# Performance work log

Hardware: AMD Instinct MI355X
Metric: run time of the kernel (lower is better)

Reference implementation:

```python
import jax, jax.numpy as jnp
import numpy as np

N = 262144      # total nodes
E = 1048576     # total edges
G = 8192        # num graphs (= batch[-1]+1)
H = 128         # hidden
L = 4           # layers
VA = 64         # atom feature vocab
VB = 8          # bond feature vocab
FA = 9          # atom feature columns
FB = 3          # bond feature columns
BN_EPS = 1e-5


def _bn(x, g, b, m, v):
    # BatchNorm1d in eval mode: running stats
    return (x - m) * jax.lax.rsqrt(v + BN_EPS) * g + b


def setup_inputs() -> dict:
    key = jax.random.key(0)
    ks = jax.random.split(key, 40)
    rn = lambda k, s, sc=0.05: jax.random.normal(k, s, dtype=jnp.float32) * sc
    x = jax.random.randint(ks[0], (N, FA), 0, VA)
    edge_index = jax.random.randint(ks[1], (2, E), 0, N)
    edge_attr = jax.random.randint(ks[2], (E, FB), 0, VB)
    batch = jnp.sort(jax.random.randint(ks[3], (N,), 0, G))
    batch = batch.at[0].set(0).at[-1].set(G - 1)
    params = dict(
        atom_emb=rn(ks[4], (FA, VA, H)),
        vn_emb=rn(ks[5], (H,)),
        bond_emb=rn(ks[6], (L, FB, VB, H)),
        conv_eps=rn(ks[7], (L,)),
        conv_W1=rn(ks[8], (L, H, 2 * H)), conv_b1=rn(ks[9], (L, 2 * H)),
        conv_bn_g=1.0 + rn(ks[10], (L, 2 * H)), conv_bn_b=rn(ks[11], (L, 2 * H)),
        conv_bn_m=rn(ks[12], (L, 2 * H), 0.1),
        conv_bn_v=0.5 + jax.random.uniform(ks[13], (L, 2 * H)) * 0.5,
        conv_W2=rn(ks[14], (L, 2 * H, H)), conv_b2=rn(ks[15], (L, H)),
        vn1_W=rn(ks[16], (L, 2 * H, 2 * H)), vn1_b=rn(ks[17], (L, 2 * H)),
        vn1_g=1.0 + rn(ks[18], (L, 2 * H)), vn1_be=rn(ks[19], (L, 2 * H)),
        vn1_m=rn(ks[20], (L, 2 * H), 0.1),
        vn1_v=0.5 + jax.random.uniform(ks[21], (L, 2 * H)) * 0.5,
        vn2_W=rn(ks[22], (L, 2 * H, H)), vn2_b=rn(ks[23], (L, H)),
        vn2_g=1.0 + rn(ks[24], (L, H)), vn2_be=rn(ks[25], (L, H)),
        vn2_m=rn(ks[26], (L, H), 0.1),
        vn2_v=0.5 + jax.random.uniform(ks[27], (L, H)) * 0.5,
        pW1=rn(ks[28], (H, H)), pb1=rn(ks[29], (H,)),
        pW2=rn(ks[30], (H, 1)), pb2=rn(ks[31], (1,)),
    )
    return dict(x=x, edge_index=edge_index, edge_attr=edge_attr, batch=batch, **params)


def reference(x, edge_index, edge_attr, batch, atom_emb, vn_emb, bond_emb,
              conv_eps, conv_W1, conv_b1, conv_bn_g, conv_bn_b, conv_bn_m, conv_bn_v,
              conv_W2, conv_b2, vn1_W, vn1_b, vn1_g, vn1_be, vn1_m, vn1_v,
              vn2_W, vn2_b, vn2_g, vn2_be, vn2_m, vn2_v, pW1, pb1, pW2, pb2):
    src, dst = edge_index[0], edge_index[1]
    # AtomEncoder: sum of per-feature embeddings -> [N, H]
    h = atom_emb[jnp.arange(FA)[:, None], x.T].sum(0)
    # virtual node embedding broadcast to all graphs: [G, H]
    vn = jnp.broadcast_to(vn_emb, (G, H))
    for i in range(L):
        h = h + vn[batch]
        # CombConv (GIN-with-edge-features): msg = relu(x_j + bond_emb)
        e = bond_emb[i][jnp.arange(FB)[:, None], edge_attr.T].sum(0)  # [E, H]
        msg = jax.nn.relu(h[src] + e)
        agg = jax.ops.segment_sum(msg, dst, num_segments=N)  # [N, H]
        z = (1.0 + conv_eps[i]) * h + agg
        z = jax.nn.relu(_bn(z @ conv_W1[i] + conv_b1[i],
                            conv_bn_g[i], conv_bn_b[i], conv_bn_m[i], conv_bn_v[i]))
        h = z @ conv_W2[i] + conv_b2[i]
        # virtual node update: gather-concat-MLP, pool, MLP
        t = jnp.concatenate([vn[batch], h], axis=-1)  # [N, 2H]
        t = jax.nn.relu(_bn(t @ vn1_W[i] + vn1_b[i],
                            vn1_g[i], vn1_be[i], vn1_m[i], vn1_v[i]))
        pooled = jax.ops.segment_sum(t, batch, num_segments=G)  # [G, 2H]
        vn = jax.nn.relu(_bn(pooled @ vn2_W[i] + vn2_b[i],
                             vn2_g[i], vn2_be[i], vn2_m[i], vn2_v[i]))
    # JK='L': last virtual-node representation; dropout=0
    out = jax.nn.relu(vn @ pW1 + pb1) @ pW2 + pb2  # [G, 1]
    return jnp.clip(out, 0.0, 50.0)  # eval-mode clamp
```

## Files before the change

### kernel.cpp

```cpp
#include <hip/hip_runtime.h>
#include <hip/hip_fp16.h>

#define NN 262144
#define EE 1048576
#define GG 8192
#define HH 128
#define FBc 3
#define VAc 64
#define VBc 8
#define FAc 9

typedef _Float16 f16;
typedef _Float16 f16x8 __attribute__((ext_vector_type(8)));
typedef float f32x4 __attribute__((ext_vector_type(4)));

__device__ __forceinline__ float h2f(ushort u) {
    __half h; *(ushort*)&h = u; return __half2float(h);
}
__device__ __forceinline__ ushort f2h(float f) {
    __half h = __float2half_rn(f); return *(ushort*)&h;
}

__global__ void k_zero(float* __restrict__ p) {
    size_t i = (size_t)(blockIdx.x * 256 + threadIdx.x) * 4;
    *(float4*)(p + i) = make_float4(0.f, 0.f, 0.f, 0.f);
}

__global__ void k_atom(const int* __restrict__ x, const float* __restrict__ emb,
                       ushort* __restrict__ h16) {
    int t = blockIdx.x * 256 + threadIdx.x;
    int n = t >> 5, c = (t & 31) << 2;
    if (n >= NN) return;
    float4 a = make_float4(0.f, 0.f, 0.f, 0.f);
#pragma unroll
    for (int f = 0; f < FAc; ++f) {
        int v = x[n * FAc + f];
        float4 e = *(const float4*)(emb + ((size_t)(f * VAc + v)) * HH + c);
        a.x += e.x; a.y += e.y; a.z += e.z; a.w += e.w;
    }
    ushort4 o;
    o.x = f2h(a.x * 0.0625f); o.y = f2h(a.y * 0.0625f);
    o.z = f2h(a.z * 0.0625f); o.w = f2h(a.w * 0.0625f);
    *(ushort4*)(h16 + (size_t)n * HH + c) = o;
}

__global__ void k_init_vn(const float* __restrict__ vn_emb, float* __restrict__ vn) {
    int t = blockIdx.x * 256 + threadIdx.x;
    int g = t >> 5, c = (t & 31) << 2;
    *(float4*)(vn + (size_t)g * HH + c) = *(const float4*)(vn_emb + c);
}

__global__ void k_hist(const int* __restrict__ ei, int* __restrict__ deg) {
    int e = blockIdx.x * 256 + threadIdx.x;
    atomicAdd(&deg[ei[EE + e]], 1);
}
__global__ void k_scan1(const int* __restrict__ deg, int* __restrict__ rowptr,
                        int* __restrict__ sums) {
    __shared__ int s[256];
    int base = blockIdx.x * 1024 + threadIdx.x * 4;
    int4 d = *(const int4*)(deg + base);
    int t = d.x + d.y + d.z + d.w;
    s[threadIdx.x] = t;
    __syncthreads();
    for (int off = 1; off < 256; off <<= 1) {
        int v = (threadIdx.x >= off) ? s[threadIdx.x - off] : 0;
        __syncthreads();
        s[threadIdx.x] += v;
        __syncthreads();
    }
    int excl = s[threadIdx.x] - t;
    int4 o; o.x = excl; o.y = excl + d.x; o.z = o.y + d.y; o.w = o.z + d.z;
    *(int4*)(rowptr + base) = o;
    if (threadIdx.x == 255) sums[blockIdx.x] = s[255];
}
__global__ void k_scan2(int* __restrict__ sums) {
    __shared__ int s[256];
    int t = sums[threadIdx.x];
    s[threadIdx.x] = t;
    __syncthreads();
    for (int off = 1; off < 256; off <<= 1) {
        int v = (threadIdx.x >= off) ? s[threadIdx.x - off] : 0;
        __syncthreads();
        s[threadIdx.x] += v;
        __syncthreads();
    }
    sums[threadIdx.x] = s[threadIdx.x] - t;
}
__global__ void k_scan3(int* __restrict__ rowptr, const int* __restrict__ sums,
                        int* __restrict__ fill) {
    int base = blockIdx.x * 1024 + threadIdx.x * 4;
    int add = sums[blockIdx.x];
    int4 r = *(const int4*)(rowptr + base);
    r.x += add; r.y += add; r.z += add; r.w += add;
    *(int4*)(rowptr + base) = r;
    *(int4*)(fill + base) = r;
    if (blockIdx.x == 0 && threadIdx.x == 0) rowptr[NN] = EE;
}
__global__ void k_scatter(const int* __restrict__ ei, const int* __restrict__ ea,
                          int* __restrict__ fill, unsigned* __restrict__ packed) {
    int e = blockIdx.x * 256 + threadIdx.x;
    int dst = ei[EE + e];
    int pos = atomicAdd(&fill[dst], 1);
    unsigned cb = (unsigned)(ea[e * 3 + 0] + ea[e * 3 + 1] * 8 + ea[e * 3 + 2] * 64);
    packed[pos] = (unsigned)ei[e] | (cb << 18);
}

__global__ void k_ctab(const float* __restrict__ bemb, float* __restrict__ ctab) {
    int t = blockIdx.x * 256 + threadIdx.x;
    int cb = t >> 5, c = (t & 31) << 2;
    int a0 = cb & 7, a1 = (cb >> 3) & 7, a2 = cb >> 6;
    float4 b0 = *(const float4*)(bemb + (size_t)(0 * VBc + a0) * HH + c);
    float4 b1 = *(const float4*)(bemb + (size_t)(1 * VBc + a1) * HH + c);
    float4 b2 = *(const float4*)(bemb + (size_t)(2 * VBc + a2) * HH + c);
    float4 o = make_float4(b0.x + b1.x + b2.x, b0.y + b1.y + b2.y,
                           b0.z + b1.z + b2.z, b0.w + b1.w + b2.w);
    *(float4*)(ctab + (size_t)cb * HH + c) = o;
}

__global__ void k_prep(const float* __restrict__ b1, const float* __restrict__ g1,
                       const float* __restrict__ be1, const float* __restrict__ m1,
                       const float* __restrict__ v1,
                       const float* __restrict__ g3, const float* __restrict__ be3,
                       const float* __restrict__ m3, const float* __restrict__ v3,
                       float* __restrict__ ZA, float* __restrict__ ZB,
                       float* __restrict__ TA, float* __restrict__ TB,
                       float* __restrict__ S3) {
    int c = threadIdx.x;
    float s1 = g1[c] * rsqrtf(v1[c] + 1e-5f);
    ZA[c] = s1;
    ZB[c] = ((b1[c] - m1[c]) * s1 + be1[c]) * 0.0625f;
    float s3 = g3[c] * rsqrtf(v3[c] + 1e-5f);
    TA[c] = 16.f * s3;
    TB[c] = be3[c] - m3[c] * s3;
    S3[c] = s3;
}

__global__ void k_wt(const float* __restrict__ W, ushort* __restrict__ Wt, int lk, int Nsrc) {
    int o = blockIdx.x * 256 + threadIdx.x;
    int K = 1 << lk;
    int c = o >> lk, k = o & (K - 1);
    Wt[o] = f2h(W[(size_t)k * Nsrc + c]);
}

__global__ void k_agg(const ushort* __restrict__ h16, const float* __restrict__ vn,
                      const int* __restrict__ batch,
                      const int* __restrict__ rowptr, const unsigned* __restrict__ packed,
                      const float* __restrict__ ctab, ushort* __restrict__ agg) {
    int n = blockIdx.x * 4 + (threadIdx.x >> 6);
    int lane = threadIdx.x & 63;
    int co = lane * 2;
    int beg = rowptr[n], end = rowptr[n + 1];
    float a0 = 0.f, a1 = 0.f;
    int i = beg;
    for (; i + 1 < end; i += 2) {
        unsigned p0 = packed[i], p1 = packed[i + 1];
        int s0 = p0 & 0x3FFFF, s1 = p1 & 0x3FFFF;
        int c0 = p0 >> 18, c1 = p1 >> 18;
        ushort2 u0 = *(const ushort2*)(h16 + (size_t)s0 * HH + co);
        ushort2 u1 = *(const ushort2*)(h16 + (size_t)s1 * HH + co);
        float2 v0 = *(const float2*)(vn + (size_t)batch[s0] * HH + co);
        float2 v1 = *(const float2*)(vn + (size_t)batch[s1] * HH + co);
        float2 t0 = *(const float2*)(ctab + (size_t)c0 * HH + co);
        float2 t1 = *(const float2*)(ctab + (size_t)c1 * HH + co);
        a0 += fmaxf(16.f * h2f(u0.x) + v0.x + t0.x, 0.f)
            + fmaxf(16.f * h2f(u1.x) + v1.x + t1.x, 0.f);
        a1 += fmaxf(16.f * h2f(u0.y) + v0.y + t0.y, 0.f)
            + fmaxf(16.f * h2f(u1.y) + v1.y + t1.y, 0.f);
    }
    if (i < end) {
        unsigned p = packed[i];
        int src = p & 0x3FFFF, cb = p >> 18;
        ushort2 u = *(const ushort2*)(h16 + (size_t)src * HH + co);
        float2 vv = *(const float2*)(vn + (size_t)batch[src] * HH + co);
        float2 ct = *(const float2*)(ctab + (size_t)cb * HH + co);
        a0 += fmaxf(16.f * h2f(u.x) + vv.x + ct.x, 0.f);
        a1 += fmaxf(16.f * h2f(u.y) + vv.y + ct.y, 0.f);
    }
    ushort2 o; o.x = f2h(a0 * 0.0625f); o.y = f2h(a1 * 0.0625f);
    *(ushort2*)(agg + (size_t)n * HH + co) = o;
}

__global__ void __launch_bounds__(512)
k_conv(ushort* __restrict__ h16, const ushort* __restrict__ agg,
       const ushort* __restrict__ W1t, const ushort* __restrict__ W2t,
       const ushort* __restrict__ W3t,
       const int* __restrict__ batch, const float* __restrict__ vn,
       const float* __restrict__ vnW,
       const float* __restrict__ eps_ptr,
       const float* __restrict__ ZA, const float* __restrict__ ZB,
       const float* __restrict__ b2,
       const float* __restrict__ TA, const float* __restrict__ TB,
       float* __restrict__ pooled) {
    __shared__ ushort As[128][128];
    __shared__ ushort zs[128][256];
    __shared__ ushort Wb[128][128];
    __shared__ int batchL[128];
    const int tid = threadIdx.x;
    const int r0 = blockIdx.x * 128;
    const int w = tid >> 6, l = tid & 63, lr = l & 15, lg = l >> 4, lr7 = lr & 7;
    if (tid < 128) batchL[tid] = batch[r0 + tid];
    const float eps1 = 1.f + eps_ptr[0];

    {
        int row = w * 16 + (l >> 2), q = l & 3, r7 = row & 7;
        int gg = batch[r0 + row];
        const ushort* hp = h16 + (size_t)(r0 + row) * HH;
        const float* vp = vn + (size_t)gg * HH;
        const ushort* ap = agg + (size_t)(r0 + row) * HH;
#pragma unroll
        for (int j4 = 0; j4 < 4; ++j4) {
            int c0 = q * 32 + j4 * 8;
            f16x8 hv = *(const f16x8*)(hp + c0);
            float4 v0 = *(const float4*)(vp + c0);
            float4 v1 = *(const float4*)(vp + c0 + 4);
            f16x8 ag = *(const f16x8*)(ap + c0);
            float vv[8] = {v0.x, v0.y, v0.z, v0.w, v1.x, v1.y, v1.z, v1.w};
            f16x8 o;
#pragma unroll
            for (int j = 0; j < 8; ++j)
                o[j] = (f16)(eps1 * ((float)hv[j] + vv[j] * 0.0625f) + (float)ag[j]);
            *(f16x8*)&As[row][((c0 >> 3) ^ r7) << 3] = o;
        }
    }

    f32x4 acc[8];
    for (int ch = 0; ch < 2; ++ch) {
        if (ch) __syncthreads();
        {
            int c = tid >> 2, q = tid & 3, c7 = c & 7;
#pragma unroll
            for (int j4 = 0; j4 < 4; ++j4) {
                int blk = q * 4 + j4;
                *(f16x8*)&Wb[c][(blk ^ c7) << 3] =
                    *(const f16x8*)(W1t + (size_t)(ch * 128 + c) * 128 + blk * 8);
            }
        }
        __syncthreads();
#pragma unroll
        for (int fc = 0; fc < 8; ++fc) acc[fc] = (f32x4){0.f, 0.f, 0.f, 0.f};
#pragma unroll
        for (int k0 = 0; k0 < 4; ++k0) {
            int sb = ((k0 * 4 + lg) ^ lr7) << 3;
            f16x8 af = *(const f16x8*)&As[w * 16 + lr][sb];
#pragma unroll
            for (int fc = 0; fc < 8; ++fc) {
                f16x8 bf = *(const f16x8*)&Wb[fc * 16 + lr][sb];
                acc[fc] = __builtin_amdgcn_mfma_f32_16x16x32_f16(af, bf, acc[fc], 0, 0, 0);
            }
        }
#pragma unroll
        for (int fc = 0; fc < 8; ++fc) {
            int col = ch * 128 + fc * 16 + lr;
            float za = ZA[col], zb = ZB[col];
#pragma unroll
            for (int reg = 0; reg < 4; ++reg) {
                int rl = w * 16 + lg * 4 + reg;
                float zv = fmaxf(acc[fc][reg] * za + zb, 0.f);
                ((ushort*)zs)[rl * 256 + ((((col >> 3) ^ (rl & 7)) << 3) | (col & 7))] = f2h(zv);
            }
        }
    }

    for (int ch2 = 0; ch2 < 2; ++ch2) {
        __syncthreads();
        {
            int c = tid >> 3, q = tid & 7, c7 = c & 7;
#pragma unroll
            for (int j4 = 0; j4 < 4; ++j4) {
                int blk = q * 4 + j4;
                *(f16x8*)((ushort*)Wb + c * 256 + ((blk ^ c7) << 3)) =
                    *(const f16x8*)(W2t + (size_t)(ch2 * 64 + c) * 256 + blk * 8);
            }
        }
        __syncthreads();
#pragma unroll
        for (int fc = 0; fc < 4; ++fc) acc[fc] = (f32x4){0.f, 0.f, 0.f, 0.f};
#pragma unroll
        for (int k0 = 0; k0 < 8; ++k0) {
            int sb = ((k0 * 4 + lg) ^ lr7) << 3;
            f16x8 af = *(const f16x8*)&zs[w * 16 + lr][sb];
#pragma unroll
            for (int fc = 0; fc < 4; ++fc) {
                f16x8 bf = *(const f16x8*)((ushort*)Wb + (fc * 16 + lr) * 256 + sb);
                acc[fc] = __builtin_amdgcn_mfma_f32_16x16x32_f16(af, bf, acc[fc], 0, 0, 0);
            }
        }
#pragma unroll
        for (int fc = 0; fc < 4; ++fc) {
            int col = ch2 * 64 + fc * 16 + lr;
            float bb = b2[col];
#pragma unroll
            for (int reg = 0; reg < 4; ++reg) {
                int rl = w * 16 + lg * 4 + reg;
                float hv = acc[fc][reg] * 16.f + bb;
                ushort hq = f2h(hv * 0.0625f);
                h16[(size_t)(r0 + rl) * HH + col] = hq;
                As[rl][(((col >> 3) ^ (rl & 7)) << 3) | (col & 7)] = hq;
            }
        }
    }

    for (int ch3 = 0; ch3 < 2; ++ch3) {
        __syncthreads();
        {
            int c = tid >> 2, q = tid & 3, c7 = c & 7;
#pragma unroll
            for (int j4 = 0; j4 < 4; ++j4) {
                int blk = q * 4 + j4;
                *(f16x8*)&Wb[c][(blk ^ c7) << 3] =
                    *(const f16x8*)(W3t + (size_t)(ch3 * 128 + c) * 128 + blk * 8);
            }
        }
        __syncthreads();
#pragma unroll
        for (int fc = 0; fc < 8; ++fc) acc[fc] = (f32x4){0.f, 0.f, 0.f, 0.f};
#pragma unroll
        for (int k0 = 0; k0 < 4; ++k0) {
            int sb = ((k0 * 4 + lg) ^ lr7) << 3;
            f16x8 af = *(const f16x8*)&As[w * 16 + lr][sb];
#pragma unroll
            for (int fc = 0; fc < 8; ++fc) {
                f16x8 bf = *(const f16x8*)&Wb[fc * 16 + lr][sb];
                acc[fc] = __builtin_amdgcn_mfma_f32_16x16x32_f16(af, bf, acc[fc], 0, 0, 0);
            }
        }
        const float* vp[4];
        int rls[4];
#pragma unroll
        for (int reg = 0; reg < 4; ++reg) {
            rls[reg] = w * 16 + lg * 4 + reg;
            vp[reg] = vnW + (size_t)batchL[rls[reg]] * 256;
        }
#pragma unroll
        for (int fc = 0; fc < 8; ++fc) {
            int colg = ch3 * 128 + fc * 16 + lr;
            float ta = TA[colg], tb = TB[colg];
#pragma unroll
            for (int reg = 0; reg < 4; ++reg) {
                int rl = rls[reg];
                float tv = fmaxf(acc[fc][reg] * ta + vp[reg][colg] + tb, 0.f);
                ((ushort*)zs)[rl * 256 + ((((colg >> 3) ^ (rl & 7)) << 3) | (colg & 7))] = f2h(tv);
            }
        }
    }
    __syncthreads();
    {
        int col = tid & 255, rs = (tid >> 8) * 64;
        float s = 0.f;
        int cur = batchL[rs];
        for (int r = rs; r < rs + 64; ++r) {
            int gg = batchL[r];
            if (gg != cur) {
                atomicAdd(&pooled[(size_t)cur * 256 + col], s);
                s = 0.f; cur = gg;
            }
            s += h2f(((const ushort*)zs)[r * 256 + ((((col >> 3) ^ (r & 7)) << 3) | (col & 7))]);
        }
        atomicAdd(&pooled[(size_t)cur * 256 + col], s);
    }
}

enum { E_BIAS = 0, E_BNRELU = 1 };
template <int EMODE>
__global__ void __launch_bounds__(256)
gemm_k(const void* __restrict__ Av, const float* __restrict__ B,
       const float* __restrict__ bias,
       const float* __restrict__ g_, const float* __restrict__ b_,
       const float* __restrict__ m_, const float* __restrict__ v_,
       const float* __restrict__ scp,
       void* __restrict__ outv, int K, int Nc) {
    __shared__ float As[64][33];
    __shared__ float Bs[32][64];
    const int tid = threadIdx.x;
    const int row0 = blockIdx.x * 64;
    const int col0 = blockIdx.y * 64;
    float acc[4][4] = {};
    const int tx = tid & 15, ty = tid >> 4;
    for (int k0 = 0; k0 < K; k0 += 32) {
#pragma unroll
        for (int p = 0; p < 2; ++p) {
            int idx = p * 256 + tid;
            {
                int r = idx >> 3, c = (idx & 7) << 2;
                size_t aoff = (size_t)(row0 + r) * K + k0 + c;
                float4 va = *(const float4*)((const float*)Av + aoff);
                As[r][c + 0] = va.x; As[r][c + 1] = va.y;
                As[r][c + 2] = va.z; As[r][c + 3] = va.w;
            }
            {
                int kr = idx >> 4, cc = (idx & 15) << 2;
                *(float4*)&Bs[kr][cc] =
                    *(const float4*)(B + (size_t)(k0 + kr) * Nc + col0 + cc);
            }
        }
        __syncthreads();
#pragma unroll
        for (int k = 0; k < 32; ++k) {
            float4 bv = *(const float4*)&Bs[k][tx << 2];
            float a0 = As[ty * 4 + 0][k];
            float a1 = As[ty * 4 + 1][k];
            float a2 = As[ty * 4 + 2][k];
            float a3 = As[ty * 4 + 3][k];
            acc[0][0] += a0 * bv.x; acc[0][1] += a0 * bv.y; acc[0][2] += a0 * bv.z; acc[0][3] += a0 * bv.w;
            acc[1][0] += a1 * bv.x; acc[1][1] += a1 * bv.y; acc[1][2] += a1 * bv.z; acc[1][3] += a1 * bv.w;
            acc[2][0] += a2 * bv.x; acc[2][1] += a2 * bv.y; acc[2][2] += a2 * bv.z; acc[2][3] += a2 * bv.w;
            acc[3][0] += a3 * bv.x; acc[3][1] += a3 * bv.y; acc[3][2] += a3 * bv.z; acc[3][3] += a3 * bv.w;
        }
        __syncthreads();
    }
#pragma unroll
    for (int j = 0; j < 4; ++j) {
        int gr = row0 + ty * 4 + j;
        float vals[4];
#pragma unroll
        for (int lx = 0; lx < 4; ++lx) {
            int gc = col0 + (tx << 2) + lx;
            float val = acc[j][lx];
            if (EMODE == E_BIAS) {
                float v = val + bias[gc];
                if (scp) v *= scp[gc];
                vals[lx] = v;
            } else {
                float y = val + bias[gc];
                float s = g_[gc] * rsqrtf(v_[gc] + 1e-5f);
                y = (y - m_[gc]) * s + b_[gc];
                vals[lx] = fmaxf(y, 0.f);
            }
        }
        *(float4*)((float*)outv + (size_t)gr * Nc + col0 + (tx << 2)) =
            make_float4(vals[0], vals[1], vals[2], vals[3]);
    }
}

__global__ void k_final(const float* __restrict__ vn, const float* __restrict__ pW1,
                        const float* __restrict__ pb1, const float* __restrict__ pW2,
                        const float* __restrict__ pb2, float* __restrict__ out) {
    int g = blockIdx.x;
    int j = threadIdx.x;
    __shared__ float vrow[HH];
    __shared__ float red[HH];
    vrow[j] = vn[(size_t)g * HH + j];
    __syncthreads();
    float acc = pb1[j];
    for (int k = 0; k < HH; ++k) acc = fmaf(vrow[k], pW1[k * HH + j], acc);
    red[j] = fmaxf(acc, 0.f) * pW2[j];
    __syncthreads();
    for (int s = 64; s > 0; s >>= 1) {
        if (j < s) red[j] += red[j + s];
        __syncthreads();
    }
    if (j == 0) out[g] = fminf(fmaxf(red[0] + pb2[0], 0.f), 50.f);
}

extern "C" void kernel_launch(void* const* d_in, const int* in_sizes, int n_in,
                              void* d_out, int out_size, void* d_ws, size_t ws_size,
                              hipStream_t stream) {
    const int*   x        = (const int*)  d_in[0];
    const int*   ei       = (const int*)  d_in[1];
    const int*   ea       = (const int*)  d_in[2];
    const int*   batch    = (const int*)  d_in[3];
    const float* atom_emb = (const float*)d_in[4];
    const float* vn_emb   = (const float*)d_in[5];
    const float* bond_emb = (const float*)d_in[6];
    const float* conv_eps = (const float*)d_in[7];
    const float* conv_W1  = (const float*)d_in[8];
    const float* conv_b1  = (const float*)d_in[9];
    const float* cbn_g    = (const float*)d_in[10];
    const float* cbn_b    = (const float*)d_in[11];
    const float* cbn_m    = (const float*)d_in[12];
    const float* cbn_v    = (const float*)d_in[13];
    const float* conv_W2  = (const float*)d_in[14];
    const float* conv_b2  = (const float*)d_in[15];
    const float* vn1_W    = (const float*)d_in[16];
    const float* vn1_b    = (const float*)d_in[17];
    const float* vn1_g    = (const float*)d_in[18];
    const float* vn1_be   = (const float*)d_in[19];
    const float* vn1_m    = (const float*)d_in[20];
    const float* vn1_v    = (const float*)d_in[21];
    const float* vn2_W    = (const float*)d_in[22];
    const float* vn2_b    = (const float*)d_in[23];
    const float* vn2_g    = (const float*)d_in[24];
    const float* vn2_be   = (const float*)d_in[25];
    const float* vn2_m    = (const float*)d_in[26];
    const float* vn2_v    = (const float*)d_in[27];
    const float* pW1      = (const float*)d_in[28];
    const float* pb1      = (const float*)d_in[29];
    const float* pW2      = (const float*)d_in[30];
    const float* pb2      = (const float*)d_in[31];

    char* base = (char*)d_ws;
    ushort*   h16    = (ushort*)base;
    ushort*   agg    = h16 + (size_t)NN * HH;
    unsigned* packed = (unsigned*)(agg + (size_t)NN * HH);
    int*      rowptr = (int*)(packed + EE);
    int*      fill   = rowptr + NN + 4;
    float*    ctab   = (float*)(fill + NN);
    int*      sums   = (int*)(ctab + 512 * HH);
    ushort*   W1t    = (ushort*)(sums + 256);
    ushort*   W2t    = W1t + 256 * 128;
    ushort*   W3t    = W2t + 128 * 256;
    float*    ZA     = (float*)(W3t + 256 * 128);
    float*    ZB     = ZA + 256;
    float*    TA     = ZB + 256;
    float*    TB     = TA + 256;
    float*    S3     = TB + 256;
    float*    vn     = S3 + 256;
    float*    vnW    = vn + (size_t)GG * HH;
    float*    pooled = vnW + (size_t)GG * 256;
    float*    out    = (float*)d_out;

    k_zero<<<256, 256, 0, stream>>>((float*)fill);
    k_hist<<<EE / 256, 256, 0, stream>>>(ei, fill);
    k_scan1<<<256, 256, 0, stream>>>(fill, rowptr, sums);
    k_scan2<<<1, 256, 0, stream>>>(sums);
    k_scan3<<<256, 256, 0, stream>>>(rowptr, sums, fill);
    k_scatter<<<EE / 256, 256, 0, stream>>>(ei, ea, fill, packed);
    k_atom<<<NN * 32 / 256, 256, 0, stream>>>(x, atom_emb, h16);
    k_init_vn<<<GG * HH / 4 / 256, 256, 0, stream>>>(vn_emb, vn);

    for (int i = 0; i < 4; ++i) {
        k_ctab<<<64, 256, 0, stream>>>(bond_emb + (size_t)i * FBc * VBc * HH, ctab);
        k_prep<<<1, 256, 0, stream>>>(
            conv_b1 + i * 256, cbn_g + i * 256, cbn_b + i * 256,
            cbn_m + i * 256, cbn_v + i * 256,
            vn1_g + i * 256, vn1_be + i * 256, vn1_m + i * 256, vn1_v + i * 256,
            ZA, ZB, TA, TB, S3);
        k_wt<<<128, 256, 0, stream>>>(conv_W1 + (size_t)i * HH * 256, W1t, 7, 256);
        k_wt<<<128, 256, 0, stream>>>(conv_W2 + (size_t)i * 256 * HH, W2t, 8, 128);
        k_wt<<<128, 256, 0, stream>>>(vn1_W + (size_t)i * 256 * 256 + 128 * 256, W3t, 7, 256);

        k_agg<<<NN / 4, 256, 0, stream>>>(h16, vn, batch, rowptr, packed, ctab, agg);

        {
            dim3 g3(GG / 64, 4);
            gemm_k<E_BIAS><<<g3, 256, 0, stream>>>(
                vn, vn1_W + (size_t)i * 256 * 256, vn1_b + i * 256,
                nullptr, nullptr, nullptr, nullptr, S3, vnW, HH, 256);
        }
        k_zero<<<GG * 256 / 4 / 256, 256, 0, stream>>>(pooled);

        k_conv<<<NN / 128, 512, 0, stream>>>(
            h16, agg, W1t, W2t, W3t, batch, vn, vnW, conv_eps + i,
            ZA, ZB, conv_b2 + i * HH, TA, TB, pooled);

        {
            dim3 g4(GG / 64, 2);
            gemm_k<E_BNRELU><<<g4, 256, 0, stream>>>(
                pooled, vn2_W + (size_t)i * 256 * HH, vn2_b + i * HH,
                vn2_g + i * HH, vn2_be + i * HH, vn2_m + i * HH, vn2_v + i * HH,
                nullptr, vn, 256, HH);
        }
    }
    k_final<<<GG, 128, 0, stream>>>(vn, pW1, pb1, pW2, pb2, out);
}
```

Measured before the change: 1.703 ms.

## Store virtual node as scaled fp16 and shrink conv tile to 64 rows

Adds a per-layer pass that converts the fp32 virtual-node table into a pre-scaled fp16 copy. The aggregation and conv kernels now gather half-width values, which cuts gather bandwidth. The fused conv kernel is retiled from 128-row blocks of 512 threads to 64-row blocks of 256 threads with two blocks per CU, and the W1 and W3 weights are staged in quarter chunks. This lowers LDS use per block and should raise occupancy, at the cost of reloading weights across twice as many blocks and some fp16 rounding of vn.

New measurement: 1.609 ms. -5.5%, faster.

```diff
diff --git a/kernel.cpp b/kernel.cpp
--- a/kernel.cpp
+++ b/kernel.cpp
@@ -48,6 +48,15 @@
     int t = blockIdx.x * 256 + threadIdx.x;
     int g = t >> 5, c = (t & 31) << 2;
     *(float4*)(vn + (size_t)g * HH + c) = *(const float4*)(vn_emb + c);
+}
+
+__global__ void k_vn16(const float* __restrict__ vn, ushort* __restrict__ vn16) {
+    int t = blockIdx.x * 256 + threadIdx.x;
+    float4 v = *(const float4*)(vn + (size_t)t * 4);
+    ushort4 o;
+    o.x = f2h(v.x * 0.0625f); o.y = f2h(v.y * 0.0625f);
+    o.z = f2h(v.z * 0.0625f); o.w = f2h(v.w * 0.0625f);
+    *(ushort4*)(vn16 + (size_t)t * 4) = o;
 }
 
 __global__ void k_hist(const int* __restrict__ ei, int* __restrict__ deg) {
@@ -142,7 +151,7 @@
     Wt[o] = f2h(W[(size_t)k * Nsrc + c]);
 }
 
-__global__ void k_agg(const ushort* __restrict__ h16, const float* __restrict__ vn,
+__global__ void k_agg(const ushort* __restrict__ h16, const ushort* __restrict__ vn16,
                       const int* __restrict__ batch,
                       const int* __restrict__ rowptr, const unsigned* __restrict__ packed,
                       const float* __restrict__ ctab, ushort* __restrict__ agg) {
@@ -158,118 +167,115 @@
         int c0 = p0 >> 18, c1 = p1 >> 18;
         ushort2 u0 = *(const ushort2*)(h16 + (size_t)s0 * HH + co);
         ushort2 u1 = *(const ushort2*)(h16 + (size_t)s1 * HH + co);
-        float2 v0 = *(const float2*)(vn + (size_t)batch[s0] * HH + co);
-        float2 v1 = *(const float2*)(vn + (size_t)batch[s1] * HH + co);
+        ushort2 w0 = *(const ushort2*)(vn16 + (size_t)batch[s0] * HH + co);
+        ushort2 w1 = *(const ushort2*)(vn16 + (size_t)batch[s1] * HH + co);
         float2 t0 = *(const float2*)(ctab + (size_t)c0 * HH + co);
         float2 t1 = *(const float2*)(ctab + (size_t)c1 * HH + co);
-        a0 += fmaxf(16.f * h2f(u0.x) + v0.x + t0.x, 0.f)
-            + fmaxf(16.f * h2f(u1.x) + v1.x + t1.x, 0.f);
-        a1 += fmaxf(16.f * h2f(u0.y) + v0.y + t0.y, 0.f)
-            + fmaxf(16.f * h2f(u1.y) + v1.y + t1.y, 0.f);
+        a0 += fmaxf(16.f * (h2f(u0.x) + h2f(w0.x)) + t0.x, 0.f)
+            + fmaxf(16.f * (h2f(u1.x) + h2f(w1.x)) + t1.x, 0.f);
+        a1 += fmaxf(16.f * (h2f(u0.y) + h2f(w0.y)) + t0.y, 0.f)
+            + fmaxf(16.f * (h2f(u1.y) + h2f(w1.y)) + t1.y, 0.f);
     }
     if (i < end) {
         unsigned p = packed[i];
         int src = p & 0x3FFFF, cb = p >> 18;
         ushort2 u = *(const ushort2*)(h16 + (size_t)src * HH + co);
-        float2 vv = *(const float2*)(vn + (size_t)batch[src] * HH + co);
+        ushort2 wv = *(const ushort2*)(vn16 + (size_t)batch[src] * HH + co);
         float2 ct = *(const float2*)(ctab + (size_t)cb * HH + co);
-        a0 += fmaxf(16.f * h2f(u.x) + vv.x + ct.x, 0.f);
-        a1 += fmaxf(16.f * h2f(u.y) + vv.y + ct.y, 0.f);
+        a0 += fmaxf(16.f * (h2f(u.x) + h2f(wv.x)) + ct.x, 0.f);
+        a1 += fmaxf(16.f * (h2f(u.y) + h2f(wv.y)) + ct.y, 0.f);
     }
     ushort2 o; o.x = f2h(a0 * 0.0625f); o.y = f2h(a1 * 0.0625f);
     *(ushort2*)(agg + (size_t)n * HH + co) = o;
 }
 
-__global__ void __launch_bounds__(512)
+__global__ void __launch_bounds__(256, 2)
 k_conv(ushort* __restrict__ h16, const ushort* __restrict__ agg,
        const ushort* __restrict__ W1t, const ushort* __restrict__ W2t,
        const ushort* __restrict__ W3t,
-       const int* __restrict__ batch, const float* __restrict__ vn,
+       const int* __restrict__ batch, const ushort* __restrict__ vn16,
        const float* __restrict__ vnW,
        const float* __restrict__ eps_ptr,
        const float* __restrict__ ZA, const float* __restrict__ ZB,
        const float* __restrict__ b2,
        const float* __restrict__ TA, const float* __restrict__ TB,
        float* __restrict__ pooled) {
-    __shared__ ushort As[128][128];
-    __shared__ ushort zs[128][256];
-    __shared__ ushort Wb[128][128];
-    __shared__ int batchL[128];
+    __shared__ ushort As[64][128];
+    __shared__ ushort zs[64][256];
+    __shared__ ushort Wb[64][256];
+    ushort(*Wq)[128] = (ushort(*)[128]) & Wb[0][0];
     const int tid = threadIdx.x;
-    const int r0 = blockIdx.x * 128;
+    const int r0 = blockIdx.x * 64;
     const int w = tid >> 6, l = tid & 63, lr = l & 15, lg = l >> 4, lr7 = lr & 7;
-    if (tid < 128) batchL[tid] = batch[r0 + tid];
     const float eps1 = 1.f + eps_ptr[0];
+    f32x4 acc[4];
 
     {
-        int row = w * 16 + (l >> 2), q = l & 3, r7 = row & 7;
+        int row = tid >> 2, q = tid & 3, r7 = row & 7;
         int gg = batch[r0 + row];
         const ushort* hp = h16 + (size_t)(r0 + row) * HH;
-        const float* vp = vn + (size_t)gg * HH;
+        const ushort* vp = vn16 + (size_t)gg * HH;
         const ushort* ap = agg + (size_t)(r0 + row) * HH;
 #pragma unroll
         for (int j4 = 0; j4 < 4; ++j4) {
             int c0 = q * 32 + j4 * 8;
             f16x8 hv = *(const f16x8*)(hp + c0);
-            float4 v0 = *(const float4*)(vp + c0);
-            float4 v1 = *(const float4*)(vp + c0 + 4);
+            f16x8 vg = *(const f16x8*)(vp + c0);
             f16x8 ag = *(const f16x8*)(ap + c0);
-            float vv[8] = {v0.x, v0.y, v0.z, v0.w, v1.x, v1.y, v1.z, v1.w};
             f16x8 o;
 #pragma unroll
             for (int j = 0; j < 8; ++j)
-                o[j] = (f16)(eps1 * ((float)hv[j] + vv[j] * 0.0625f) + (float)ag[j]);
+                o[j] = (f16)(eps1 * ((float)hv[j] + (float)vg[j]) + (float)ag[j]);
             *(f16x8*)&As[row][((c0 >> 3) ^ r7) << 3] = o;
         }
     }
 
-    f32x4 acc[8];
-    for (int ch = 0; ch < 2; ++ch) {
-        if (ch) __syncthreads();
+    for (int qt = 0; qt < 4; ++qt) {
+        __syncthreads();
         {
             int c = tid >> 2, q = tid & 3, c7 = c & 7;
 #pragma unroll
             for (int j4 = 0; j4 < 4; ++j4) {
                 int blk = q * 4 + j4;
-                *(f16x8*)&Wb[c][(blk ^ c7) << 3] =
-                    *(const f16x8*)(W1t + (size_t)(ch * 128 + c) * 128 + blk * 8);
-            }
-        }
-        __syncthreads();
-#pragma unroll
-        for (int fc = 0; fc < 8; ++fc) acc[fc] = (f32x4){0.f, 0.f, 0.f, 0.f};
+                *(f16x8*)&Wq[c][(blk ^ c7) << 3] =
+                    *(const f16x8*)(W1t + (size_t)(qt * 64 + c) * 128 + blk * 8);
+            }
+        }
+        __syncthreads();
+#pragma unroll
+        for (int fc = 0; fc < 4; ++fc) acc[fc] = (f32x4){0.f, 0.f, 0.f, 0.f};
 #pragma unroll
         for (int k0 = 0; k0 < 4; ++k0) {
             int sb = ((k0 * 4 + lg) ^ lr7) << 3;
             f16x8 af = *(const f16x8*)&As[w * 16 + lr][sb];
 #pragma unroll
-            for (int fc = 0; fc < 8; ++fc) {
-                f16x8 bf = *(const f16x8*)&Wb[fc * 16 + lr][sb];
+            for (int fc = 0; fc < 4; ++fc) {
+                f16x8 bf = *(const f16x8*)&Wq[fc * 16 + lr][sb];
                 acc[fc] = __builtin_amdgcn_mfma_f32_16x16x32_f16(af, bf, acc[fc], 0, 0, 0);
             }
         }
 #pragma unroll
-        for (int fc = 0; fc < 8; ++fc) {
-            int col = ch * 128 + fc * 16 + lr;
+        for (int fc = 0; fc < 4; ++fc) {
+            int col = qt * 64 + fc * 16 + lr;
             float za = ZA[col], zb = ZB[col];
 #pragma unroll
             for (int reg = 0; reg < 4; ++reg) {
                 int rl = w * 16 + lg * 4 + reg;
                 float zv = fmaxf(acc[fc][reg] * za + zb, 0.f);
-                ((ushort*)zs)[rl * 256 + ((((col >> 3) ^ (rl & 7)) << 3) | (col & 7))] = f2h(zv);
-            }
-        }
-    }
-
-    for (int ch2 = 0; ch2 < 2; ++ch2) {
+                zs[rl][(((col >> 3) ^ (rl & 7)) << 3) | (col & 7)] = f2h(zv);
+            }
+        }
+    }
+
+    for (int ch = 0; ch < 2; ++ch) {
         __syncthreads();
         {
-            int c = tid >> 3, q = tid & 7, c7 = c & 7;
-#pragma unroll
-            for (int j4 = 0; j4 < 4; ++j4) {
-                int blk = q * 4 + j4;
-                *(f16x8*)((ushort*)Wb + c * 256 + ((blk ^ c7) << 3)) =
-                    *(const f16x8*)(W2t + (size_t)(ch2 * 64 + c) * 256 + blk * 8);
+            int c = tid >> 2, q = tid & 3, c7 = c & 7;
+#pragma unroll
+            for (int j8 = 0; j8 < 8; ++j8) {
+                int blk = q * 8 + j8;
+                *(f16x8*)&Wb[c][(blk ^ c7) << 3] =
+                    *(const f16x8*)(W2t + (size_t)(ch * 64 + c) * 256 + blk * 8);
             }
         }
         __syncthreads();
@@ -281,13 +287,13 @@
             f16x8 af = *(const f16x8*)&zs[w * 16 + lr][sb];
 #pragma unroll
             for (int fc = 0; fc < 4; ++fc) {
-                f16x8 bf = *(const f16x8*)((ushort*)Wb + (fc * 16 + lr) * 256 + sb);
+                f16x8 bf = *(const f16x8*)&Wb[fc * 16 + lr][sb];
                 acc[fc] = __builtin_amdgcn_mfma_f32_16x16x32_f16(af, bf, acc[fc], 0, 0, 0);
             }
         }
 #pragma unroll
         for (int fc = 0; fc < 4; ++fc) {
-            int col = ch2 * 64 + fc * 16 + lr;
+            int col = ch * 64 + fc * 16 + lr;
             float bb = b2[col];
 #pragma unroll
             for (int reg = 0; reg < 4; ++reg) {
@@ -300,61 +306,60 @@
         }
     }
 
-    for (int ch3 = 0; ch3 < 2; ++ch3) {
+    for (int qt = 0; qt < 4; ++qt) {
         __syncthreads();
         {
             int c = tid >> 2, q = tid & 3, c7 = c & 7;
 #pragma unroll
             for (int j4 = 0; j4 < 4; ++j4) {
                 int blk = q * 4 + j4;
-                *(f16x8*)&Wb[c][(blk ^ c7) << 3] =
-                    *(const f16x8*)(W3t + (size_t)(ch3 * 128 + c) * 128 + blk * 8);
-            }
-        }
-        __syncthreads();
-#pragma unroll
-        for (int fc = 0; fc < 8; ++fc) acc[fc] = (f32x4){0.f, 0.f, 0.f, 0.f};
+                *(f16x8*)&Wq[c][(blk ^ c7) << 3] =
+                    *(const f16x8*)(W3t + (size_t)(qt * 64 + c) * 128 + blk * 8);
+            }
+        }
+        __syncthreads();
+#pragma unroll
+        for (int fc = 0; fc < 4; ++fc) acc[fc] = (f32x4){0.f, 0.f, 0.f, 0.f};
 #pragma unroll
         for (int k0 = 0; k0 < 4; ++k0) {
             int sb = ((k0 * 4 + lg) ^ lr7) << 3;
             f16x8 af = *(const f16x8*)&As[w * 16 + lr][sb];
 #pragma unroll
-            for (int fc = 0; fc < 8; ++fc) {
-                f16x8 bf = *(const f16x8*)&Wb[fc * 16 + lr][sb];
+            for (int fc = 0; fc < 4; ++fc) {
+                f16x8 bf = *(const f16x8*)&Wq[fc * 16 + lr][sb];
                 acc[fc] = __builtin_amdgcn_mfma_f32_16x16x32_f16(af, bf, acc[fc], 0, 0, 0);
             }
         }
-        const float* vp[4];
-        int rls[4];
+        int rls[4], ggs[4];
 #pragma unroll
         for (int reg = 0; reg < 4; ++reg) {
             rls[reg] = w * 16 + lg * 4 + reg;
-            vp[reg] = vnW + (size_t)batchL[rls[reg]] * 256;
-        }
-#pragma unroll
-        for (int fc = 0; fc < 8; ++fc) {
-            int colg = ch3 * 128 + fc * 16 + lr;
+            ggs[reg] = batch[r0 + rls[reg]];
+        }
+#pragma unroll
+        for (int fc = 0; fc < 4; ++fc) {
+            int colg = qt * 64 + fc * 16 + lr;
             float ta = TA[colg], tb = TB[colg];
 #pragma unroll
             for (int reg = 0; reg < 4; ++reg) {
                 int rl = rls[reg];
-                float tv = fmaxf(acc[fc][reg] * ta + vp[reg][colg] + tb, 0.f);
-                ((ushort*)zs)[rl * 256 + ((((colg >> 3) ^ (rl & 7)) << 3) | (colg & 7))] = f2h(tv);
+                float tv = fmaxf(acc[fc][reg] * ta + vnW[(size_t)ggs[reg] * 256 + colg] + tb, 0.f);
+                zs[rl][(((colg >> 3) ^ (rl & 7)) << 3) | (colg & 7)] = f2h(tv);
             }
         }
     }
     __syncthreads();
     {
-        int col = tid & 255, rs = (tid >> 8) * 64;
+        int col = tid;
         float s = 0.f;
-        int cur = batchL[rs];
-        for (int r = rs; r < rs + 64; ++r) {
-            int gg = batchL[r];
+        int cur = batch[r0];
+        for (int r = 0; r < 64; ++r) {
+            int gg = batch[r0 + r];
             if (gg != cur) {
                 atomicAdd(&pooled[(size_t)cur * 256 + col], s);
                 s = 0.f; cur = gg;
             }
-            s += h2f(((const ushort*)zs)[r * 256 + ((((col >> 3) ^ (r & 7)) << 3) | (col & 7))]);
+            s += h2f(zs[r][(((col >> 3) ^ (r & 7)) << 3) | (col & 7)]);
         }
         atomicAdd(&pooled[(size_t)cur * 256 + col], s);
     }
@@ -505,7 +510,8 @@
     float*    TB     = TA + 256;
     float*    S3     = TB + 256;
     float*    vn     = S3 + 256;
-    float*    vnW    = vn + (size_t)GG * HH;
+    ushort*   vn16   = (ushort*)(vn + (size_t)GG * HH);
+    float*    vnW    = (float*)(vn16 + (size_t)GG * HH);
     float*    pooled = vnW + (size_t)GG * 256;
     float*    out    = (float*)d_out;
 
@@ -528,8 +534,9 @@
         k_wt<<<128, 256, 0, stream>>>(conv_W1 + (size_t)i * HH * 256, W1t, 7, 256);
         k_wt<<<128, 256, 0, stream>>>(conv_W2 + (size_t)i * 256 * HH, W2t, 8, 128);
         k_wt<<<128, 256, 0, stream>>>(vn1_W + (size_t)i * 256 * 256 + 128 * 256, W3t, 7, 256);
-
-        k_agg<<<NN / 4, 256, 0, stream>>>(h16, vn, batch, rowptr, packed, ctab, agg);
+        k_vn16<<<GG * HH / 4 / 256, 256, 0, stream>>>(vn, vn16);
+
+        k_agg<<<NN / 4, 256, 0, stream>>>(h16, vn16, batch, rowptr, packed, ctab, agg);
 
         {
             dim3 g3(GG / 64, 4);
@@ -539,8 +546,8 @@
         }
         k_zero<<<GG * 256 / 4 / 256, 256, 0, stream>>>(pooled);
 
-        k_conv<<<NN / 128, 512, 0, stream>>>(
-            h16, agg, W1t, W2t, W3t, batch, vn, vnW, conv_eps + i,
+        k_conv<<<NN / 64, 256, 0, stream>>>(
+            h16, agg, W1t, W2t, W3t, batch, vn16, vnW, conv_eps + i,
             ZA, ZB, conv_b2 + i * HH, TA, TB, pooled);
 
         {
```
